# Kernel tuning notes

Measured on AMD Instinct MI355X. Metric: run time of the kernel, lower is better.

## Reference

```python
import jax, jax.numpy as jnp
import numpy as np

DIM = 768
H = 12
HD = 64  # head_dim = dim // num_heads
SCALE = HD ** (-0.5)
EPS = 1e-6


def setup_inputs() -> dict:
    key = jax.random.key(0)
    k1, k2, k3, k4, k5 = jax.random.split(key, 5)
    B, N = 8, 1024
    x = jax.random.normal(k1, (B, N, DIM), dtype=jnp.float32)
    policy = jax.random.uniform(k2, (B, N, 1), dtype=jnp.float32)
    # nn.Linear weights: [out_features, in_features]; qkv_bias=False, proj has bias
    qkv_w = jax.random.normal(k3, (3 * H * HD, DIM), dtype=jnp.float32) * (DIM ** -0.5)
    proj_w = jax.random.normal(k4, (DIM, H * HD), dtype=jnp.float32) * ((H * HD) ** -0.5)
    proj_b = jax.random.normal(k5, (DIM,), dtype=jnp.float32) * 0.01
    return {"x": x, "policy": policy, "qkv_w": qkv_w, "proj_w": proj_w, "proj_b": proj_b}


def _softmax_with_policy(attn, policy):
    # attn: [B,H,N,N], policy: [B,N,1]
    B, Hh, N, _ = attn.shape
    attn_policy = policy.reshape(B, 1, 1, N)
    eye = jnp.eye(N, dtype=attn_policy.dtype).reshape(1, 1, N, N)
    attn_policy = attn_policy + (1.0 - attn_policy) * eye
    max_att = jnp.max(attn, axis=-1, keepdims=True)
    a = jnp.exp((attn - max_att).astype(jnp.float32)) * attn_policy.astype(jnp.float32)
    a = (a + EPS / N) / (jnp.sum(a, axis=-1, keepdims=True) + EPS)
    return a.astype(max_att.dtype)


def reference(x, policy, qkv_w, proj_w, proj_b):
    B, N, C = x.shape
    qkv = (x @ qkv_w.T).reshape(B, N, 3, H, HD)
    qkv = jnp.transpose(qkv, (2, 0, 3, 1, 4))  # [3,B,H,N,HD]
    q, k, v = qkv[0], qkv[1], qkv[2]
    attn = jnp.einsum('bhnd,bhmd->bhnm', q * SCALE, k)  # [B,H,N,N]
    attn = _softmax_with_policy(attn, policy)
    out = jnp.einsum('bhnm,bhmd->bhnd', attn, v)  # [B,H,N,HD]
    out = jnp.transpose(out, (0, 2, 1, 3)).reshape(B, N, H * HD)
    return out @ proj_w.T + proj_b
```

## Files before the change

kernel.cpp:

```cpp
#include <hip/hip_runtime.h>

typedef __bf16 bf16x8 __attribute__((ext_vector_type(8)));
typedef float floatx4 __attribute__((ext_vector_type(4)));

#define EPSF 1e-6f

__device__ inline unsigned short f2bf(float f) {
  union { float f; unsigned u; } x; x.f = f;
  unsigned r = x.u + 0x7FFFu + ((x.u >> 16) & 1u);
  return (unsigned short)(r >> 16);
}
__device__ inline float bf2f(unsigned short u) {
  union { unsigned u; float f; } x; x.u = ((unsigned)u) << 16;
  return x.f;
}
__device__ inline unsigned pk2bf(float lo, float hi) {
  union { float f; unsigned u; } a, b; a.f = lo; b.f = hi;
  unsigned ua = a.u + 0x8000u, ub = b.u + 0x8000u;
  return (ub & 0xFFFF0000u) | (ua >> 16);
}
__device__ inline float fexp2(float x) { return __builtin_amdgcn_exp2f(x); }

__device__ inline floatx4 mfma16(bf16x8 a, bf16x8 b, floatx4 c) {
  return __builtin_amdgcn_mfma_f32_16x16x32_bf16(a, b, c, 0, 0, 0);
}

__device__ inline void gll16(const unsigned short* g, unsigned short* l) {
  __builtin_amdgcn_global_load_lds((__attribute__((address_space(1))) void*)g,
                                   (__attribute__((address_space(3))) void*)l, 16, 0, 0);
}

__device__ __host__ inline int sigma_inv(int p) {
  const int qq = p >> 3, jj = p & 7;
  return (jj < 4) ? (qq * 4 + jj) : (16 + qq * 4 + jj - 4);
}

__global__ __launch_bounds__(256) void prep_kernel(const float* __restrict__ x,
                                                   const float* __restrict__ qkv_w,
                                                   const float* __restrict__ proj_w,
                                                   const float* __restrict__ policy,
                                                   unsigned short* __restrict__ xb,
                                                   unsigned short* __restrict__ wqkv,
                                                   unsigned short* __restrict__ wproj,
                                                   unsigned short* __restrict__ pbf) {
  const int bid = blockIdx.x, tid = threadIdx.x;
  if (bid < 3072) {
    const int i = bid * 2048 + tid * 8;
    float4 v0 = *(const float4*)(x + i);
    float4 v1 = *(const float4*)(x + i + 4);
    __align__(16) unsigned short o[8] = {f2bf(v0.x), f2bf(v0.y), f2bf(v0.z), f2bf(v0.w),
                                         f2bf(v1.x), f2bf(v1.y), f2bf(v1.z), f2bf(v1.w)};
    *(float4*)(xb + i) = *(float4*)o;
  } else if (bid < 3936) {
    const int i = (bid - 3072) * 2048 + tid * 8;
    const float s = (i < 589824) ? 0.18033688011112042f : 1.0f;
    float4 v0 = *(const float4*)(qkv_w + i);
    float4 v1 = *(const float4*)(qkv_w + i + 4);
    __align__(16) unsigned short o[8] = {
        f2bf(v0.x * s), f2bf(v0.y * s), f2bf(v0.z * s), f2bf(v0.w * s),
        f2bf(v1.x * s), f2bf(v1.y * s), f2bf(v1.z * s), f2bf(v1.w * s)};
    *(float4*)(wqkv + i) = *(float4*)o;
  } else if (bid < 4224) {
    const int i0 = (bid - 3936) * 2048 + tid * 8;
    const int base = (i0 / 768) * 768 + ((i0 % 768) & ~63);
    __align__(16) unsigned short o[8];
#pragma unroll
    for (int t = 0; t < 8; t++) {
      const int cp = (i0 + t) & 63;
      const int c = 16 * (cp & 3) + (cp >> 2);
      o[t] = f2bf(proj_w[base + c]);
    }
    *(float4*)(wproj + i0) = *(float4*)o;
  } else {
    const int idx = (bid - 4224) * 256 + tid;
    const int b = idx >> 10, g = idx & 1023;
    const int c = ((g >> 5) << 5) + sigma_inv(g & 31);
    pbf[idx] = f2bf(policy[b * 1024 + c]);
  }
}

template <int EP, int BN, int W>
__global__ __launch_bounds__(256, W) void gemm_bt(const unsigned short* __restrict__ A,
                                                  const unsigned short* __restrict__ Bt,
                                                  void* __restrict__ Cout,
                                                  const float* __restrict__ bias,
                                                  int M, int N, int K) {
  constexpr int J = BN / 32;
  __shared__ __align__(16) unsigned short sA[128 * 64];
  __shared__ __align__(16) unsigned short sB[BN * 64];
  const int bid = blockIdx.x;
  const int yb = (bid & 7) * 8 + ((bid >> 3) & 7);
  const int xb_ = bid >> 6;
  const int m0 = yb * 128, n0 = xb_ * BN;
  const int tid = threadIdx.x;
  const int lane = tid & 63, wave = tid >> 6;
  const int qd = lane >> 4, l15 = lane & 15;
  const int wr = (wave >> 1) * 64, wc = (wave & 1) * (BN / 2);
  const int srow = tid >> 3;
  const int scb = (tid & 7) ^ (srow & 7);
  const unsigned short* Ag = A + (long)(m0 + srow) * K + scb * 8;
  const unsigned short* Bg = Bt + (long)(n0 + srow) * K + scb * 8;
  const int x7 = l15 & 7;
  floatx4 acc[4][J] = {};
  for (int k0 = 0; k0 < K; k0 += 64) {
    __syncthreads();
#pragma unroll
    for (int p = 0; p < 4; p++) gll16(Ag + (long)(p * 32) * K + k0, sA + p * 2048 + wave * 512);
#pragma unroll
    for (int p = 0; p < J; p++) gll16(Bg + (long)(p * 32) * K + k0, sB + p * 2048 + wave * 512);
    __syncthreads();
#pragma unroll
    for (int s = 0; s < 2; s++) {
      const int cw = ((s * 4 + qd) ^ x7) * 8;
      bf16x8 af[4], bf[J];
#pragma unroll
      for (int i = 0; i < 4; i++) af[i] = *(const bf16x8*)&sA[(wr + i * 16 + l15) * 64 + cw];
#pragma unroll
      for (int j = 0; j < J; j++) bf[j] = *(const bf16x8*)&sB[(wc + j * 16 + l15) * 64 + cw];
#pragma unroll
      for (int i = 0; i < 4; i++)
#pragma unroll
        for (int j = 0; j < J; j++) acc[i][j] = mfma16(af[i], bf[j], acc[i][j]);
    }
  }
  if constexpr (EP == 0) {
#pragma unroll
    for (int i = 0; i < 4; i++)
#pragma unroll
      for (int r = 0; r < 4; r++) {
        const int row = m0 + wr + i * 16 + qd * 4 + r;
        __align__(8) unsigned short pk[4];
#pragma unroll
        for (int j = 0; j < 4; j++) pk[j] = f2bf(acc[i][j][r]);
        *(uint2*)((unsigned short*)Cout + (long)row * N + n0 + wc + 4 * l15) = *(uint2*)pk;
      }
  } else {
#pragma unroll
    for (int i = 0; i < 4; i++)
#pragma unroll
      for (int j = 0; j < J; j++) {
        const int col = n0 + wc + j * 16 + l15;
#pragma unroll
        for (int r = 0; r < 4; r++) {
          const int row = m0 + wr + i * 16 + qd * 4 + r;
          ((float*)Cout)[(long)row * N + col] = acc[i][j][r] + bias[col];
        }
      }
  }
}

__global__ __launch_bounds__(256) void transpose_v(const unsigned short* __restrict__ qkv,
                                                   const float* __restrict__ policy,
                                                   unsigned short* __restrict__ vTp) {
  __shared__ unsigned short tile[64][72];
  __shared__ float sPol[64];
  const int bh = blockIdx.y;
  const int b = bh / 12, h = bh % 12;
  const int n0 = blockIdx.x * 64;
  const int t = threadIdx.x;
  if (t < 64) sPol[t] = policy[b * 1024 + n0 + t];
  {
    const int nr = t >> 2, dc = (t & 3) * 16;
    const unsigned short* src = qkv + (long)(b * 1024 + n0 + nr) * 2304 + 2 * 768 + h * 64 + dc;
    float4 v0 = *(const float4*)src;
    float4 v1 = *(const float4*)(src + 8);
    *(float4*)&tile[nr][dc] = v0;
    *(float4*)&tile[nr][dc + 8] = v1;
  }
  __syncthreads();
  {
    const int d = t >> 2, nc = (t & 3) * 16;
    __align__(16) unsigned short o[16];
#pragma unroll
    for (int jj = 0; jj < 16; jj++) {
      const int cc = nc + jj;
      const int cl = (cc & 32) + sigma_inv(cc & 31);
      o[jj] = f2bf(bf2f(tile[cl][d]) * sPol[cl]);
    }
    unsigned short* dst = vTp + (long)(bh * 64 + d) * 1024 + n0 + nc;
    *(float4*)dst = *(float4*)&o[0];
    *(float4*)(dst + 8) = *(float4*)&o[8];
  }
}

__global__ __launch_bounds__(256, 6) void attn_kernel(const unsigned short* __restrict__ qkv,
                                                      const unsigned short* __restrict__ vTp,
                                                      const unsigned short* __restrict__ pbf,
                                                      const float* __restrict__ policy,
                                                      unsigned short* __restrict__ aout) {
  __shared__ __align__(16) unsigned short sK[2][2048];
  __shared__ __align__(16) unsigned short sV[2][2048];
  __shared__ __align__(16) unsigned short sPv[1024];
  __shared__ float sD[4][16];
  const int bid = blockIdx.x;
  const int bh = bid % 96, qt = bid / 96;
  const int b = bh / 12, h = bh % 12;
  const int tid = threadIdx.x;
  const int wave = tid >> 6, lane = tid & 63;
  const int qd = lane >> 4, l15 = lane & 15;
  const int q0 = qt * 64 + wave * 16;
  const unsigned short* qb = qkv + (long)(b * 1024 + q0 + l15) * 2304 + h * 64 + qd * 8;
  bf16x8 qf0 = *(const bf16x8*)qb;
  bf16x8 qf1 = *(const bf16x8*)(qb + 32);
  if (tid < 128) *(float4*)(sPv + tid * 8) = *(const float4*)(pbf + b * 1024 + tid * 8);
  const int krow = wave * 8 + (lane >> 3);
  const int kcb = (lane & 7) ^ (lane >> 3);
  const unsigned short* kgl = qkv + (long)(b * 1024 + krow) * 2304 + 768 + h * 64 + kcb * 8;
  const int vrow = tid >> 2;
  const int vcb = (tid & 3) ^ ((vrow ^ (vrow >> 2)) & 3);
  const unsigned short* vgl = vTp + (long)(bh * 64 + vrow) * 1024 + vcb * 8;
  const int x7 = l15 & 7;
  const int vsw = (qd ^ ((l15 ^ (l15 >> 2)) & 3)) * 8;
  floatx4 O[4] = {};
  floatx4 Dl = {};
  const floatx4 z = {0.f, 0.f, 0.f, 0.f};
  gll16(kgl, &sK[0][wave * 512]);
  gll16(vgl, &sV[0][wave * 512]);
  __builtin_amdgcn_s_waitcnt(0);
  __syncthreads();
  for (int it = 0; it < 32; ++it) {
    const int buf = it & 1;
    if (it < 31) {
      gll16(kgl + (long)(32 * (it + 1)) * 2304, &sK[buf ^ 1][wave * 512]);
      gll16(vgl + 32 * (it + 1), &sV[buf ^ 1][wave * 512]);
    }
    bf16x8 k00 = *(const bf16x8*)&sK[buf][(0 * 16 + l15) * 64 + ((0 + qd) ^ x7) * 8];
    bf16x8 k01 = *(const bf16x8*)&sK[buf][(0 * 16 + l15) * 64 + ((4 + qd) ^ x7) * 8];
    bf16x8 k10 = *(const bf16x8*)&sK[buf][(1 * 16 + l15) * 64 + ((0 + qd) ^ x7) * 8];
    bf16x8 k11 = *(const bf16x8*)&sK[buf][(1 * 16 + l15) * 64 + ((4 + qd) ^ x7) * 8];
    bf16x8 pv = *(const bf16x8*)&sPv[it * 32 + qd * 8];
    floatx4 tA = mfma16(k01, qf1, mfma16(k00, qf0, z));
    floatx4 tB = mfma16(k11, qf1, mfma16(k10, qf0, z));
    uint4 pu;
    pu.x = pk2bf(fexp2(tA[0]), fexp2(tA[1]));
    pu.y = pk2bf(fexp2(tA[2]), fexp2(tA[3]));
    pu.z = pk2bf(fexp2(tB[0]), fexp2(tB[1]));
    pu.w = pk2bf(fexp2(tB[2]), fexp2(tB[3]));
    bf16x8 pf = *(bf16x8*)&pu;
    bf16x8 vf0 = *(const bf16x8*)&sV[buf][(0 * 16 + l15) * 32 + vsw];
    bf16x8 vf1 = *(const bf16x8*)&sV[buf][(1 * 16 + l15) * 32 + vsw];
    bf16x8 vf2 = *(const bf16x8*)&sV[buf][(2 * 16 + l15) * 32 + vsw];
    bf16x8 vf3 = *(const bf16x8*)&sV[buf][(3 * 16 + l15) * 32 + vsw];
    Dl = mfma16(pf, pv, Dl);
    O[0] = mfma16(pf, vf0, O[0]);
    O[1] = mfma16(pf, vf1, O[1]);
    O[2] = mfma16(pf, vf2, O[2]);
    O[3] = mfma16(pf, vf3, O[3]);
    __builtin_amdgcn_s_waitcnt(0);
    __syncthreads();
  }
  {
    const unsigned short* kd = qkv + (long)(b * 1024 + q0 + l15) * 2304 + 768 + h * 64 + qd * 8;
    bf16x8 kd0 = *(const bf16x8*)kd;
    bf16x8 kd1 = *(const bf16x8*)(kd + 32);
    float part = 0.f;
#pragma unroll
    for (int jj = 0; jj < 8; jj++)
      part += (float)qf0[jj] * (float)kd0[jj] + (float)qf1[jj] * (float)kd1[jj];
    part += __shfl_xor(part, 16);
    part += __shfl_xor(part, 32);
    if (qd == 0) {
      const float p0 = policy[b * 1024 + q0 + l15];
      sD[wave][l15] = fexp2(part) * (1.0f - p0);
    }
    __builtin_amdgcn_s_waitcnt(0);
    const unsigned short* vdiag = qkv + (long)(b * 1024 + q0) * 2304 + 1536 + h * 64 + l15;
#pragma unroll
    for (int r = 0; r < 4; r++) {
      const int row = qd * 4 + r;
      const float cv = sD[wave][row];
#pragma unroll
      for (int j = 0; j < 4; j++)
        O[j][r] += cv * bf2f(vdiag[(long)row * 2304 + j * 16]);
      Dl[r] += cv;
    }
  }
  const long ob = (long)(b * 1024 + q0 + qd * 4) * 768 + h * 64 + l15;
#pragma unroll
  for (int r = 0; r < 4; r++) {
    const float li = 1.0f / (Dl[r] + EPSF);
#pragma unroll
    for (int j = 0; j < 4; j++)
      aout[ob + (long)r * 768 + j * 16] = f2bf(O[j][r] * li);
  }
}

extern "C" void kernel_launch(void* const* d_in, const int* in_sizes, int n_in,
                              void* d_out, int out_size, void* d_ws, size_t ws_size,
                              hipStream_t stream) {
  const float* x      = (const float*)d_in[0];
  const float* policy = (const float*)d_in[1];
  const float* qkv_w  = (const float*)d_in[2];
  const float* proj_w = (const float*)d_in[3];
  const float* proj_b = (const float*)d_in[4];
  float* out = (float*)d_out;

  char* ws = (char*)d_ws;
  unsigned short* xb    = (unsigned short*)(ws + 0);
  unsigned short* wqkv  = (unsigned short*)(ws + 12582912);
  unsigned short* wproj = (unsigned short*)(ws + 16121856);
  unsigned short* qkvb  = (unsigned short*)(ws + 17301504);
  unsigned short* vTp   = (unsigned short*)(ws + 55050240);
  unsigned short* aoutb = (unsigned short*)(ws + 67633152);
  unsigned short* pbf   = (unsigned short*)(ws + 80216064);

  prep_kernel<<<4256, 256, 0, stream>>>(x, qkv_w, proj_w, policy, xb, wqkv, wproj, pbf);
  gemm_bt<0, 128, 4><<<dim3(18 * 64), 256, 0, stream>>>(xb, wqkv, qkvb, nullptr, 8192, 2304, 768);
  transpose_v<<<dim3(16, 96), 256, 0, stream>>>(qkvb, policy, vTp);
  attn_kernel<<<dim3(1536), 256, 0, stream>>>(qkvb, vTp, pbf, policy, aoutb);
  gemm_bt<1, 64, 3><<<dim3(12 * 64), 256, 0, stream>>>(aoutb, wproj, out, proj_b, 8192, 768, 768);
}
```

Baseline: 180.3 us.

## Give each wave private K/V double buffers and drop per-iteration block barriers

Each wave now loads its own full K and V tiles into private LDS double buffers instead of sharing one block-wide tile. This removes the __syncthreads per key tile and replaces the full waitcnt(0) with a partial vmcnt wait, so loads and MFMAs from different waves can overlap. The policy vector is read from global memory into registers one step ahead rather than staged in LDS. The cost is 4x the K/V LDS and global/L2 load traffic, and launch bounds drop from 6 to 2 blocks per CU, which reduces occupancy.

```diff
diff --git a/kernel.cpp b/kernel.cpp
--- a/kernel.cpp
+++ b/kernel.cpp
@@ -183,14 +183,13 @@
   }
 }
 
-__global__ __launch_bounds__(256, 6) void attn_kernel(const unsigned short* __restrict__ qkv,
+__global__ __launch_bounds__(256, 2) void attn_kernel(const unsigned short* __restrict__ qkv,
                                                       const unsigned short* __restrict__ vTp,
                                                       const unsigned short* __restrict__ pbf,
                                                       const float* __restrict__ policy,
                                                       unsigned short* __restrict__ aout) {
-  __shared__ __align__(16) unsigned short sK[2][2048];
-  __shared__ __align__(16) unsigned short sV[2][2048];
-  __shared__ __align__(16) unsigned short sPv[1024];
+  __shared__ __align__(16) unsigned short sK[4][2][2048];
+  __shared__ __align__(16) unsigned short sV[4][2][2048];
   __shared__ float sD[4][16];
   const int bid = blockIdx.x;
   const int bh = bid % 96, qt = bid / 96;
@@ -202,33 +201,48 @@
   const unsigned short* qb = qkv + (long)(b * 1024 + q0 + l15) * 2304 + h * 64 + qd * 8;
   bf16x8 qf0 = *(const bf16x8*)qb;
   bf16x8 qf1 = *(const bf16x8*)(qb + 32);
-  if (tid < 128) *(float4*)(sPv + tid * 8) = *(const float4*)(pbf + b * 1024 + tid * 8);
-  const int krow = wave * 8 + (lane >> 3);
   const int kcb = (lane & 7) ^ (lane >> 3);
-  const unsigned short* kgl = qkv + (long)(b * 1024 + krow) * 2304 + 768 + h * 64 + kcb * 8;
-  const int vrow = tid >> 2;
-  const int vcb = (tid & 3) ^ ((vrow ^ (vrow >> 2)) & 3);
-  const unsigned short* vgl = vTp + (long)(bh * 64 + vrow) * 1024 + vcb * 8;
+  const unsigned short* kgl = qkv + (long)(b * 1024 + (lane >> 3)) * 2304 + 768 + h * 64 + kcb * 8;
+  const int r16 = lane >> 2;
+  const int vcb = (lane & 3) ^ ((r16 ^ (r16 >> 2)) & 3);
+  const unsigned short* vgl = vTp + (long)(bh * 64 + r16) * 1024 + vcb * 8;
+  unsigned short* myK = &sK[wave][0][0];
+  unsigned short* myV = &sV[wave][0][0];
   const int x7 = l15 & 7;
   const int vsw = (qd ^ ((l15 ^ (l15 >> 2)) & 3)) * 8;
+  const unsigned short* pvg = pbf + b * 1024 + qd * 8;
   floatx4 O[4] = {};
   floatx4 Dl = {};
   const floatx4 z = {0.f, 0.f, 0.f, 0.f};
-  gll16(kgl, &sK[0][wave * 512]);
-  gll16(vgl, &sV[0][wave * 512]);
-  __builtin_amdgcn_s_waitcnt(0);
-  __syncthreads();
+  bf16x8 pvn = *(const bf16x8*)pvg;
+#pragma unroll
+  for (int p = 0; p < 4; p++) gll16(kgl + (long)(p * 8) * 2304, myK + p * 512);
+#pragma unroll
+  for (int p = 0; p < 4; p++) gll16(vgl + (long)(p * 16) * 1024, myV + p * 512);
+  __builtin_amdgcn_s_waitcnt(0x0F70);
   for (int it = 0; it < 32; ++it) {
     const int buf = it & 1;
+    bf16x8 pv = pvn;
     if (it < 31) {
-      gll16(kgl + (long)(32 * (it + 1)) * 2304, &sK[buf ^ 1][wave * 512]);
-      gll16(vgl + 32 * (it + 1), &sV[buf ^ 1][wave * 512]);
-    }
-    bf16x8 k00 = *(const bf16x8*)&sK[buf][(0 * 16 + l15) * 64 + ((0 + qd) ^ x7) * 8];
-    bf16x8 k01 = *(const bf16x8*)&sK[buf][(0 * 16 + l15) * 64 + ((4 + qd) ^ x7) * 8];
-    bf16x8 k10 = *(const bf16x8*)&sK[buf][(1 * 16 + l15) * 64 + ((0 + qd) ^ x7) * 8];
-    bf16x8 k11 = *(const bf16x8*)&sK[buf][(1 * 16 + l15) * 64 + ((4 + qd) ^ x7) * 8];
-    bf16x8 pv = *(const bf16x8*)&sPv[it * 32 + qd * 8];
+      const int cn = (it + 1) * 32;
+      pvn = *(const bf16x8*)(pvg + cn);
+      unsigned short* dK = myK + (buf ^ 1) * 2048;
+      unsigned short* dV = myV + (buf ^ 1) * 2048;
+#pragma unroll
+      for (int p = 0; p < 4; p++) gll16(kgl + (long)(cn + p * 8) * 2304, dK + p * 512);
+#pragma unroll
+      for (int p = 0; p < 4; p++) gll16(vgl + (long)(p * 16) * 1024 + cn, dV + p * 512);
+      __builtin_amdgcn_s_waitcnt(0x0F79);
+    } else {
+      __builtin_amdgcn_s_waitcnt(0x0F70);
+    }
+    __builtin_amdgcn_sched_barrier(0);
+    const unsigned short* kb = myK + buf * 2048;
+    const unsigned short* vb = myV + buf * 2048;
+    bf16x8 k00 = *(const bf16x8*)&kb[(0 * 16 + l15) * 64 + ((0 + qd) ^ x7) * 8];
+    bf16x8 k01 = *(const bf16x8*)&kb[(0 * 16 + l15) * 64 + ((4 + qd) ^ x7) * 8];
+    bf16x8 k10 = *(const bf16x8*)&kb[(1 * 16 + l15) * 64 + ((0 + qd) ^ x7) * 8];
+    bf16x8 k11 = *(const bf16x8*)&kb[(1 * 16 + l15) * 64 + ((4 + qd) ^ x7) * 8];
     floatx4 tA = mfma16(k01, qf1, mfma16(k00, qf0, z));
     floatx4 tB = mfma16(k11, qf1, mfma16(k10, qf0, z));
     uint4 pu;
@@ -237,17 +251,15 @@
     pu.z = pk2bf(fexp2(tB[0]), fexp2(tB[1]));
     pu.w = pk2bf(fexp2(tB[2]), fexp2(tB[3]));
     bf16x8 pf = *(bf16x8*)&pu;
-    bf16x8 vf0 = *(const bf16x8*)&sV[buf][(0 * 16 + l15) * 32 + vsw];
-    bf16x8 vf1 = *(const bf16x8*)&sV[buf][(1 * 16 + l15) * 32 + vsw];
-    bf16x8 vf2 = *(const bf16x8*)&sV[buf][(2 * 16 + l15) * 32 + vsw];
-    bf16x8 vf3 = *(const bf16x8*)&sV[buf][(3 * 16 + l15) * 32 + vsw];
+    bf16x8 vf0 = *(const bf16x8*)&vb[(0 * 16 + l15) * 32 + vsw];
+    bf16x8 vf1 = *(const bf16x8*)&vb[(1 * 16 + l15) * 32 + vsw];
+    bf16x8 vf2 = *(const bf16x8*)&vb[(2 * 16 + l15) * 32 + vsw];
+    bf16x8 vf3 = *(const bf16x8*)&vb[(3 * 16 + l15) * 32 + vsw];
     Dl = mfma16(pf, pv, Dl);
     O[0] = mfma16(pf, vf0, O[0]);
     O[1] = mfma16(pf, vf1, O[1]);
     O[2] = mfma16(pf, vf2, O[2]);
     O[3] = mfma16(pf, vf3, O[3]);
-    __builtin_amdgcn_s_waitcnt(0);
-    __syncthreads();
   }
   {
     const unsigned short* kd = qkv + (long)(b * 1024 + q0 + l15) * 2304 + 768 + h * 64 + qd * 8;
```

Result: slower. 210.5 us (+16.8%).
